# Kernel tuning notes

Hardware: AMD Instinct MI355X
Metric: run time of the kernel (lower is better)

The kernel has to match this reference:

```python
import jax, jax.numpy as jnp
import numpy as np

B, T, C = 2, 2048, 1024
H = 16
D = C // H  # head_dim = 64


def setup_inputs() -> dict:
    key = jax.random.key(0)
    k1, k2, k3, k4 = jax.random.split(key, 4)
    x = jax.random.normal(k1, (B, T, C), dtype=jnp.float32)
    # parameter scales ~ torch default init magnitude
    w_qkv = jax.random.normal(k2, (C, 3 * C), dtype=jnp.float32) * (1.0 / np.sqrt(C))
    w_proj = jax.random.normal(k3, (C, C), dtype=jnp.float32) * (1.0 / np.sqrt(C))
    b_proj = jax.random.normal(k4, (C,), dtype=jnp.float32) * 0.01
    return {"x": x, "w_qkv": w_qkv, "w_proj": w_proj, "b_proj": b_proj}


def reference(x, w_qkv, w_proj, b_proj):
    b, t, c = x.shape
    scale = 1.0 / jnp.sqrt(jnp.asarray(D, dtype=x.dtype))
    qkv = x @ w_qkv                                   # [B,T,3C]
    q, k, v = jnp.split(qkv, 3, axis=-1)
    def heads(u):  # [B,T,C] -> [B,H,T,D]
        return u.reshape(b, t, H, D).transpose(0, 2, 1, 3)
    q, k, v = heads(q), heads(k), heads(v)
    attn = jnp.einsum('bhqd,bhkd->bhqk', q, k) * scale  # [B,H,T,T]
    causal = jnp.tril(jnp.ones((t, t), dtype=bool))
    attn = jnp.where(causal, attn, -jnp.inf)
    attn = jax.nn.softmax(attn, axis=-1)
    # dropout p=0.0 / eval mode: identity
    out = jnp.einsum('bhqk,bhkd->bhqd', attn, v)        # [B,H,T,D]
    out = out.transpose(0, 2, 1, 3).reshape(b, t, c)
    return out @ w_proj + b_proj
```

## Files before the change

### kernel.cpp

```cpp
#include <hip/hip_runtime.h>
#include <stdint.h>

#define Bn 2
#define Tn 2048
#define Cn 1024
#define Hn 16
#define Dn 64
#define Mn (Bn*Tn)

typedef __attribute__((ext_vector_type(8))) short bf16x8;
typedef __attribute__((ext_vector_type(4))) float f32x4;
typedef __attribute__((ext_vector_type(4))) unsigned int u32x4;
typedef __attribute__((ext_vector_type(2))) unsigned int u32x2;
typedef unsigned short u16;

__device__ __forceinline__ u16 f2bf(float f) {
  union { float f; uint32_t u; } v; v.f = f;
  uint32_t u = v.u;
  return (u16)((u + 0x7fffu + ((u >> 16) & 1u)) >> 16);
}

__device__ __forceinline__ uint32_t pk_bf16(float lo, float hi) {
  uint32_t r;
  asm volatile("v_cvt_pk_bf16_f32 %0, %1, %2" : "=v"(r) : "v"(lo), "v"(hi));
  return r;
}

__device__ __forceinline__ void async16(const void* g, void* lds) {
  __builtin_amdgcn_global_load_lds((const __attribute__((address_space(1))) void*)g,
                                   (__attribute__((address_space(3))) void*)lds,
                                   16, 0, 0);
}


__global__ void cvt_x(const float* __restrict__ x, u16* __restrict__ xb) {
  int i = (blockIdx.x * 256 + threadIdx.x) * 4;
  float4 v = *(const float4*)(x + i);
  ushort4 o;
  o.x = f2bf(v.x); o.y = f2bf(v.y); o.z = f2bf(v.z); o.w = f2bf(v.w);
  *(ushort4*)(xb + i) = o;
}

template<int K, int N>
__global__ void cvt_T(const float* __restrict__ in, u16* __restrict__ out) {
  __shared__ float tile[32][33];
  int n0 = blockIdx.x * 32, k0 = blockIdx.y * 32;
  int tx = threadIdx.x & 31, ty = threadIdx.x >> 5;
  #pragma unroll
  for (int i = 0; i < 32; i += 8)
    tile[ty + i][tx] = in[(size_t)(k0 + ty + i) * N + n0 + tx];
  __syncthreads();
  #pragma unroll
  for (int i = 0; i < 32; i += 8)
    out[(size_t)(n0 + ty + i) * K + k0 + tx] = f2bf(tile[tx][ty + i]);
}


template<int EPI>
__launch_bounds__(256, 2)
__global__ void gemm_bt(const u16* __restrict__ A, const u16* __restrict__ Bt, int N,
                        u16* __restrict__ Qb, u16* __restrict__ Kb, u16* __restrict__ Vb,
                        float* __restrict__ Out, const float* __restrict__ bias) {
  constexpr int Kd = 1024;
  __shared__ u16 As[128][64];
  __shared__ u16 Bs[128][64];
  const int nT = N >> 7;
  const int m0 = (blockIdx.x / nT) << 7;
  const int n0 = (blockIdx.x % nT) << 7;
  const int tid = threadIdx.x;
  const int lane = tid & 63, wid = tid >> 6;
  const int wr = wid >> 1, wc = wid & 1;
  const int lr = lane & 15, lg = lane >> 4;

  f32x4 acc[4][4] = {};

  for (int kb = 0; kb < Kd; kb += 64) {
    #pragma unroll
    for (int i = 0; i < 4; ++i) {
      int c = (wid * 4 + i) * 64 + lane;
      int row = c >> 3, ko = (c & 7) << 3;
      async16(A + (size_t)(m0 + row) * Kd + kb + ko, &As[0][0] + c * 8);
      async16(Bt + (size_t)(n0 + row) * Kd + kb + ko, &Bs[0][0] + c * 8);
    }
    __syncthreads();
    bf16x8 af[2][4], bf[2][4];
    #pragma unroll
    for (int kc = 0; kc < 2; ++kc) {
      #pragma unroll
      for (int mi = 0; mi < 4; ++mi) {
        af[kc][mi] = *(const bf16x8*)&As[wr * 64 + mi * 16 + lr][kc * 32 + lg * 8];
        bf[kc][mi] = *(const bf16x8*)&Bs[wc * 64 + mi * 16 + lr][kc * 32 + lg * 8];
      }
    }
    #pragma unroll
    for (int kc = 0; kc < 2; ++kc)
      #pragma unroll
      for (int mi = 0; mi < 4; ++mi)
        #pragma unroll
        for (int ni = 0; ni < 4; ++ni)
          acc[mi][ni] = __builtin_amdgcn_mfma_f32_16x16x32_bf16(af[kc][mi], bf[kc][ni], acc[mi][ni], 0, 0, 0);
    __syncthreads();
  }

  if constexpr (EPI == 0) {
    #pragma unroll
    for (int mi = 0; mi < 4; ++mi) {
      int r0 = m0 + wr * 64 + mi * 16 + lg * 4;
      int bb = r0 >> 11;
      int t0 = r0 & 2047;
      #pragma unroll
      for (int ni = 0; ni < 4; ++ni) {
        int col = n0 + wc * 64 + ni * 16 + lr;
        int sel = col >> 10, rem = col & 1023;
        int h = rem >> 6, d = rem & 63;
        f32x4 v = acc[mi][ni];
        if (sel == 0) {
          size_t base = ((size_t)(bb * Hn + h) * Tn + t0) * Dn + d;
          #pragma unroll
          for (int r = 0; r < 4; ++r) Qb[base + (size_t)r * Dn] = f2bf(v[r] * 0.125f);
        } else if (sel == 1) {
          size_t base = ((size_t)(bb * Hn + h) * Tn + t0) * Dn + d;
          #pragma unroll
          for (int r = 0; r < 4; ++r) Kb[base + (size_t)r * Dn] = f2bf(v[r]);
        } else {
          size_t base = ((size_t)(bb * Hn + h) * Dn + d) * Tn + t0;
          ushort4 o;
          o.x = f2bf(v[0]); o.y = f2bf(v[1]); o.z = f2bf(v[2]); o.w = f2bf(v[3]);
          *(ushort4*)(Vb + base) = o;
        }
      }
    }
  } else {
    #pragma unroll
    for (int mi = 0; mi < 4; ++mi) {
      int r0 = m0 + wr * 64 + mi * 16 + lg * 4;
      #pragma unroll
      for (int ni = 0; ni < 4; ++ni) {
        int col = n0 + wc * 64 + ni * 16 + lr;
        float bv = bias[col];
        #pragma unroll
        for (int r = 0; r < 4; ++r)
          Out[(size_t)(r0 + r) * Cn + col] = acc[mi][ni][r] + bv;
      }
    }
  }
}


__device__ __forceinline__ void stage_kv(const u16* __restrict__ K,
                                         const u16* __restrict__ Vt, int k0,
                                         u16* __restrict__ Kbuf, u16* __restrict__ Vbuf,
                                         int tid) {
  #pragma unroll
  for (int i = 0; i < 2; ++i) {
    int c = i * 256 + tid;
    int row = c >> 3;
    int js = (c & 7) ^ (row & 7);
    async16(K + (size_t)(k0 + row) * Dn + js * 8, Kbuf + c * 8);
    async16(Vt + (size_t)row * Tn + k0 + js * 8, Vbuf + c * 8);
  }
}

__launch_bounds__(256, 2)
__global__ void attn(const u16* __restrict__ Qb, const u16* __restrict__ Kb,
                     const u16* __restrict__ Vb, u16* __restrict__ Ob) {
  __shared__ u16 __attribute__((aligned(16))) Ks[2 * 4096];
  __shared__ u16 __attribute__((aligned(16))) Vs[2 * 4096];
  __shared__ uint32_t __attribute__((aligned(16))) P32[4][16][36];

  const int x = blockIdx.x;
  const int wg = (x & 7) * 64 + (x >> 3);
  const int bh = wg >> 4;
  const int a  = wg & 15;
  const int tid = threadIdx.x;
  const int lane = tid & 63, wid = tid >> 6;
  const int lr = lane & 15, lg = lane >> 4;
  const int bb = bh >> 4, h = bh & 15;

  const u16* Q  = Qb + (size_t)bh * Tn * Dn;
  const u16* K  = Kb + (size_t)bh * Tn * Dn;
  const u16* Vt = Vb + (size_t)bh * Dn * Tn;

  const int swz = (lr & 7);
  const int qoff = wid * 16 + lr;
  const int koff0 = lg * 4;

  #pragma unroll 1
  for (int g = 0; g < 2; ++g) {
    const int q0 = (g == 0 ? (31 - a) : a) * 64;
    const int nt = (q0 >> 6) + 1;

    bf16x8 qf[2];
    qf[0] = *(const bf16x8*)(Q + (size_t)(q0 + qoff) * Dn + lg * 8);
    qf[1] = *(const bf16x8*)(Q + (size_t)(q0 + qoff) * Dn + 32 + lg * 8);

    f32x4 o[4] = {};
    float m = -1e30f, l = 0.f;

    int cur = 0;
    stage_kv(K, Vt, 0, Ks, Vs, tid);
    __syncthreads();

    for (int t = 0; t < nt; ++t) {
      if (t + 1 < nt)
        stage_kv(K, Vt, (t + 1) << 6,
                 Ks + (cur ^ 1) * 4096, Vs + (cur ^ 1) * 4096, tid);

      const u16* Kc = Ks + cur * 4096;
      const u16* Vc = Vs + cur * 4096;

      f32x4 s[4] = {};
      __builtin_amdgcn_s_setprio(1);
      #pragma unroll
      for (int f = 0; f < 4; ++f) {
        const int row = f * 16 + lr;
        #pragma unroll
        for (int kc = 0; kc < 2; ++kc) {
          bf16x8 kf = *(const bf16x8*)(Kc + row * 64 + (((kc * 4 + lg) ^ swz) * 8));
          s[f] = __builtin_amdgcn_mfma_f32_16x16x32_bf16(kf, qf[kc], s[f], 0, 0, 0);
        }
      }
      __builtin_amdgcn_s_setprio(0);

      if (t == nt - 1) {
        #pragma unroll
        for (int f = 0; f < 4; ++f)
          #pragma unroll
          for (int r = 0; r < 4; ++r)
            if (f * 16 + koff0 + r > qoff) s[f][r] = -1e30f;
      }

      float pm = fmaxf(fmaxf(fmaxf(s[0][0], s[0][1]), fmaxf(s[0][2], s[0][3])),
                       fmaxf(fmaxf(s[1][0], s[1][1]), fmaxf(s[1][2], s[1][3])));
      float pm2 = fmaxf(fmaxf(fmaxf(s[2][0], s[2][1]), fmaxf(s[2][2], s[2][3])),
                        fmaxf(fmaxf(s[3][0], s[3][1]), fmaxf(s[3][2], s[3][3])));
      pm = fmaxf(pm, pm2);
      pm = fmaxf(pm, __shfl_xor(pm, 16));
      pm = fmaxf(pm, __shfl_xor(pm, 32));

      if (!__all(pm - m <= 8.f)) {
        float mn = fmaxf(m, pm);
        float fac = __expf(m - mn);
        l *= fac;
        #pragma unroll
        for (int f = 0; f < 4; ++f) {
          o[f][0] *= fac; o[f][1] *= fac; o[f][2] *= fac; o[f][3] *= fac;
        }
        m = mn;
      }

      float sum = 0.f;
      #pragma unroll
      for (int f = 0; f < 4; ++f) {
        #pragma unroll
        for (int r = 0; r < 4; ++r) {
          float p = __expf(s[f][r] - m);
          s[f][r] = p;
          sum += p;
        }
      }
      sum += __shfl_xor(sum, 16);
      sum += __shfl_xor(sum, 32);
      l += sum;

      #pragma unroll
      for (int f = 0; f < 4; ++f) {
        u32x2 w;
        w.x = pk_bf16(s[f][0], s[f][1]);
        w.y = pk_bf16(s[f][2], s[f][3]);
        *(u32x2*)&P32[wid][lr][f * 8 + lg * 2] = w;
      }

      __builtin_amdgcn_s_setprio(1);
      #pragma unroll
      for (int kc = 0; kc < 2; ++kc) {
        u32x4 p4 = *(const u32x4*)&P32[wid][lr][kc * 16 + lg * 4];
        bf16x8 pf = __builtin_bit_cast(bf16x8, p4);
        #pragma unroll
        for (int f = 0; f < 4; ++f) {
          const int row = f * 16 + lr;
          bf16x8 vf = *(const bf16x8*)(Vc + row * 64 + (((kc * 4 + lg) ^ swz) * 8));
          o[f] = __builtin_amdgcn_mfma_f32_16x16x32_bf16(vf, pf, o[f], 0, 0, 0);
        }
      }
      __builtin_amdgcn_s_setprio(0);

      __syncthreads();
      cur ^= 1;
    }

    float inv = 1.f / l;
    #pragma unroll
    for (int f = 0; f < 4; ++f) {
      u32x2 w;
      w.x = pk_bf16(o[f][0] * inv, o[f][1] * inv);
      w.y = pk_bf16(o[f][2] * inv, o[f][3] * inv);
      *(u32x2*)&P32[wid][lr][f * 8 + lg * 2] = w;
    }
    u32x4 r0 = *(const u32x4*)&P32[wid][lr][lg * 8];
    u32x4 r1 = *(const u32x4*)&P32[wid][lr][lg * 8 + 4];
    u16* obase = Ob + ((size_t)(bb * Tn + q0 + qoff)) * Cn + h * Dn + lg * 16;
    *(u32x4*)(obase) = r0;
    *(u32x4*)(obase + 8) = r1;
    __syncthreads();
  }
}


extern "C" void kernel_launch(void* const* d_in, const int* in_sizes, int n_in,
                              void* d_out, int out_size, void* d_ws, size_t ws_size,
                              hipStream_t stream) {
  const float* x = (const float*)d_in[0];
  const float* w_qkv = (const float*)d_in[1];
  const float* w_proj = (const float*)d_in[2];
  const float* b_proj = (const float*)d_in[3];
  float* out = (float*)d_out;
  char* ws = (char*)d_ws;

  u16* xb     = (u16*)(ws);
  u16* wqkvT  = (u16*)(ws + (size_t)( 8u << 20));
  u16* wprojT = (u16*)(ws + (size_t)(14u << 20));
  u16* Qb     = (u16*)(ws + (size_t)(16u << 20));
  u16* Kb     = (u16*)(ws + (size_t)(24u << 20));
  u16* Vb     = (u16*)(ws + (size_t)(32u << 20));

  cvt_x<<<dim3(4096), dim3(256), 0, stream>>>(x, xb);
  cvt_T<1024, 3072><<<dim3(96, 32), dim3(256), 0, stream>>>(w_qkv, wqkvT);
  cvt_T<1024, 1024><<<dim3(32, 32), dim3(256), 0, stream>>>(w_proj, wprojT);

  gemm_bt<0><<<dim3(32 * 24), dim3(256), 0, stream>>>(xb, wqkvT, 3072,
                                                      Qb, Kb, Vb, nullptr, nullptr);
  attn<<<dim3(512), dim3(256), 0, stream>>>(Qb, Kb, Vb, xb );
  gemm_bt<1><<<dim3(32 * 8), dim3(256), 0, stream>>>(xb, wprojT, 1024,
                                                     nullptr, nullptr, nullptr, out, b_proj);
}
```

Before: 122.2 us.

## Load V directly to registers, split attention grid per query tile, raise occupancy

The attention kernel no longer stages V through shared memory; each wave loads its V fragments straight from global memory into registers, which halves the LDS footprint. Launch bounds go from 2 to 4 blocks per CU, and the grid doubles to one block per (batch-head, query tile) instead of pairing long and short tiles in one block. Blocks are ordered longest-first and grouped so that each XCD handles four heads. The intent is more concurrent waves to hide latency, at the cost of redundant uncoalesced global V reads across the four waves and more register pressure.

```diff
diff --git a/kernel.cpp b/kernel.cpp
--- a/kernel.cpp
+++ b/kernel.cpp
@@ -147,31 +147,31 @@
 }
 
 
-__device__ __forceinline__ void stage_kv(const u16* __restrict__ K,
-                                         const u16* __restrict__ Vt, int k0,
-                                         u16* __restrict__ Kbuf, u16* __restrict__ Vbuf,
-                                         int tid) {
+__device__ __forceinline__ void stage_k(const u16* __restrict__ K, int k0,
+                                        u16* __restrict__ Kbuf, int tid) {
   #pragma unroll
   for (int i = 0; i < 2; ++i) {
     int c = i * 256 + tid;
     int row = c >> 3;
     int js = (c & 7) ^ (row & 7);
     async16(K + (size_t)(k0 + row) * Dn + js * 8, Kbuf + c * 8);
-    async16(Vt + (size_t)row * Tn + k0 + js * 8, Vbuf + c * 8);
-  }
-}
-
-__launch_bounds__(256, 2)
+  }
+}
+
+__launch_bounds__(256, 4)
 __global__ void attn(const u16* __restrict__ Qb, const u16* __restrict__ Kb,
                      const u16* __restrict__ Vb, u16* __restrict__ Ob) {
   __shared__ u16 __attribute__((aligned(16))) Ks[2 * 4096];
-  __shared__ u16 __attribute__((aligned(16))) Vs[2 * 4096];
   __shared__ uint32_t __attribute__((aligned(16))) P32[4][16][36];
 
-  const int x = blockIdx.x;
-  const int wg = (x & 7) * 64 + (x >> 3);
-  const int bh = wg >> 4;
-  const int a  = wg & 15;
+  const int raw = blockIdx.x;
+  const int xcd = raw & 7;
+  const int idx = raw >> 3;
+  const int bh  = xcd * 4 + (idx & 3);
+  const int qt  = 31 - (idx >> 2);
+  const int q0  = qt * 64;
+  const int nt  = qt + 1;
+
   const int tid = threadIdx.x;
   const int lane = tid & 63, wid = tid >> 6;
   const int lr = lane & 15, lg = lane >> 4;
@@ -185,125 +185,121 @@
   const int qoff = wid * 16 + lr;
   const int koff0 = lg * 4;
 
-  #pragma unroll 1
-  for (int g = 0; g < 2; ++g) {
-    const int q0 = (g == 0 ? (31 - a) : a) * 64;
-    const int nt = (q0 >> 6) + 1;
-
-    bf16x8 qf[2];
-    qf[0] = *(const bf16x8*)(Q + (size_t)(q0 + qoff) * Dn + lg * 8);
-    qf[1] = *(const bf16x8*)(Q + (size_t)(q0 + qoff) * Dn + 32 + lg * 8);
-
-    f32x4 o[4] = {};
-    float m = -1e30f, l = 0.f;
-
-    int cur = 0;
-    stage_kv(K, Vt, 0, Ks, Vs, tid);
-    __syncthreads();
-
-    for (int t = 0; t < nt; ++t) {
-      if (t + 1 < nt)
-        stage_kv(K, Vt, (t + 1) << 6,
-                 Ks + (cur ^ 1) * 4096, Vs + (cur ^ 1) * 4096, tid);
-
-      const u16* Kc = Ks + cur * 4096;
-      const u16* Vc = Vs + cur * 4096;
-
-      f32x4 s[4] = {};
-      __builtin_amdgcn_s_setprio(1);
+  bf16x8 qf[2];
+  qf[0] = *(const bf16x8*)(Q + (size_t)(q0 + qoff) * Dn + lg * 8);
+  qf[1] = *(const bf16x8*)(Q + (size_t)(q0 + qoff) * Dn + 32 + lg * 8);
+
+  f32x4 o[4] = {};
+  float m = -1e30f, l = 0.f;
+
+  int cur = 0;
+  stage_k(K, 0, Ks, tid);
+  __syncthreads();
+
+  for (int t = 0; t < nt; ++t) {
+    const int k0 = t << 6;
+    if (t + 1 < nt)
+      stage_k(K, (t + 1) << 6, Ks + (cur ^ 1) * 4096, tid);
+
+    bf16x8 vf[2][4];
+    #pragma unroll
+    for (int kc = 0; kc < 2; ++kc)
+      #pragma unroll
+      for (int f = 0; f < 4; ++f)
+        vf[kc][f] = *(const bf16x8*)(Vt + (size_t)(f * 16 + lr) * Tn + k0 + kc * 32 + lg * 8);
+
+    const u16* Kc = Ks + cur * 4096;
+
+    f32x4 s[4] = {};
+    __builtin_amdgcn_s_setprio(1);
+    #pragma unroll
+    for (int f = 0; f < 4; ++f) {
+      const int row = f * 16 + lr;
+      #pragma unroll
+      for (int kc = 0; kc < 2; ++kc) {
+        bf16x8 kf = *(const bf16x8*)(Kc + row * 64 + (((kc * 4 + lg) ^ swz) * 8));
+        s[f] = __builtin_amdgcn_mfma_f32_16x16x32_bf16(kf, qf[kc], s[f], 0, 0, 0);
+      }
+    }
+    __builtin_amdgcn_s_setprio(0);
+
+    if (t == nt - 1) {
+      #pragma unroll
+      for (int f = 0; f < 4; ++f)
+        #pragma unroll
+        for (int r = 0; r < 4; ++r)
+          if (f * 16 + koff0 + r > qoff) s[f][r] = -1e30f;
+    }
+
+    float pm = fmaxf(fmaxf(fmaxf(s[0][0], s[0][1]), fmaxf(s[0][2], s[0][3])),
+                     fmaxf(fmaxf(s[1][0], s[1][1]), fmaxf(s[1][2], s[1][3])));
+    float pm2 = fmaxf(fmaxf(fmaxf(s[2][0], s[2][1]), fmaxf(s[2][2], s[2][3])),
+                      fmaxf(fmaxf(s[3][0], s[3][1]), fmaxf(s[3][2], s[3][3])));
+    pm = fmaxf(pm, pm2);
+    pm = fmaxf(pm, __shfl_xor(pm, 16));
+    pm = fmaxf(pm, __shfl_xor(pm, 32));
+
+    if (!__all(pm - m <= 8.f)) {
+      float mn = fmaxf(m, pm);
+      float fac = __expf(m - mn);
+      l *= fac;
       #pragma unroll
       for (int f = 0; f < 4; ++f) {
-        const int row = f * 16 + lr;
-        #pragma unroll
-        for (int kc = 0; kc < 2; ++kc) {
-          bf16x8 kf = *(const bf16x8*)(Kc + row * 64 + (((kc * 4 + lg) ^ swz) * 8));
-          s[f] = __builtin_amdgcn_mfma_f32_16x16x32_bf16(kf, qf[kc], s[f], 0, 0, 0);
-        }
-      }
-      __builtin_amdgcn_s_setprio(0);
-
-      if (t == nt - 1) {
-        #pragma unroll
-        for (int f = 0; f < 4; ++f)
-          #pragma unroll
-          for (int r = 0; r < 4; ++r)
-            if (f * 16 + koff0 + r > qoff) s[f][r] = -1e30f;
-      }
-
-      float pm = fmaxf(fmaxf(fmaxf(s[0][0], s[0][1]), fmaxf(s[0][2], s[0][3])),
-                       fmaxf(fmaxf(s[1][0], s[1][1]), fmaxf(s[1][2], s[1][3])));
-      float pm2 = fmaxf(fmaxf(fmaxf(s[2][0], s[2][1]), fmaxf(s[2][2], s[2][3])),
-                        fmaxf(fmaxf(s[3][0], s[3][1]), fmaxf(s[3][2], s[3][3])));
-      pm = fmaxf(pm, pm2);
-      pm = fmaxf(pm, __shfl_xor(pm, 16));
-      pm = fmaxf(pm, __shfl_xor(pm, 32));
-
-      if (!__all(pm - m <= 8.f)) {
-        float mn = fmaxf(m, pm);
-        float fac = __expf(m - mn);
-        l *= fac;
-        #pragma unroll
-        for (int f = 0; f < 4; ++f) {
-          o[f][0] *= fac; o[f][1] *= fac; o[f][2] *= fac; o[f][3] *= fac;
-        }
-        m = mn;
-      }
-
-      float sum = 0.f;
-      #pragma unroll
-      for (int f = 0; f < 4; ++f) {
-        #pragma unroll
-        for (int r = 0; r < 4; ++r) {
-          float p = __expf(s[f][r] - m);
-          s[f][r] = p;
-          sum += p;
-        }
-      }
-      sum += __shfl_xor(sum, 16);
-      sum += __shfl_xor(sum, 32);
-      l += sum;
-
-      #pragma unroll
-      for (int f = 0; f < 4; ++f) {
-        u32x2 w;
-        w.x = pk_bf16(s[f][0], s[f][1]);
-        w.y = pk_bf16(s[f][2], s[f][3]);
-        *(u32x2*)&P32[wid][lr][f * 8 + lg * 2] = w;
-      }
-
-      __builtin_amdgcn_s_setprio(1);
-      #pragma unroll
-      for (int kc = 0; kc < 2; ++kc) {
-        u32x4 p4 = *(const u32x4*)&P32[wid][lr][kc * 16 + lg * 4];
-        bf16x8 pf = __builtin_bit_cast(bf16x8, p4);
-        #pragma unroll
-        for (int f = 0; f < 4; ++f) {
-          const int row = f * 16 + lr;
-          bf16x8 vf = *(const bf16x8*)(Vc + row * 64 + (((kc * 4 + lg) ^ swz) * 8));
-          o[f] = __builtin_amdgcn_mfma_f32_16x16x32_bf16(vf, pf, o[f], 0, 0, 0);
-        }
-      }
-      __builtin_amdgcn_s_setprio(0);
-
-      __syncthreads();
-      cur ^= 1;
-    }
-
-    float inv = 1.f / l;
+        o[f][0] *= fac; o[f][1] *= fac; o[f][2] *= fac; o[f][3] *= fac;
+      }
+      m = mn;
+    }
+
+    float sum = 0.f;
+    #pragma unroll
+    for (int f = 0; f < 4; ++f) {
+      #pragma unroll
+      for (int r = 0; r < 4; ++r) {
+        float p = __expf(s[f][r] - m);
+        s[f][r] = p;
+        sum += p;
+      }
+    }
+    sum += __shfl_xor(sum, 16);
+    sum += __shfl_xor(sum, 32);
+    l += sum;
+
     #pragma unroll
     for (int f = 0; f < 4; ++f) {
       u32x2 w;
-      w.x = pk_bf16(o[f][0] * inv, o[f][1] * inv);
-      w.y = pk_bf16(o[f][2] * inv, o[f][3] * inv);
+      w.x = pk_bf16(s[f][0], s[f][1]);
+      w.y = pk_bf16(s[f][2], s[f][3]);
       *(u32x2*)&P32[wid][lr][f * 8 + lg * 2] = w;
     }
-    u32x4 r0 = *(const u32x4*)&P32[wid][lr][lg * 8];
-    u32x4 r1 = *(const u32x4*)&P32[wid][lr][lg * 8 + 4];
-    u16* obase = Ob + ((size_t)(bb * Tn + q0 + qoff)) * Cn + h * Dn + lg * 16;
-    *(u32x4*)(obase) = r0;
-    *(u32x4*)(obase + 8) = r1;
+
+    __builtin_amdgcn_s_setprio(1);
+    #pragma unroll
+    for (int kc = 0; kc < 2; ++kc) {
+      u32x4 p4 = *(const u32x4*)&P32[wid][lr][kc * 16 + lg * 4];
+      bf16x8 pf = __builtin_bit_cast(bf16x8, p4);
+      #pragma unroll
+      for (int f = 0; f < 4; ++f)
+        o[f] = __builtin_amdgcn_mfma_f32_16x16x32_bf16(vf[kc][f], pf, o[f], 0, 0, 0);
+    }
+    __builtin_amdgcn_s_setprio(0);
+
     __syncthreads();
-  }
+    cur ^= 1;
+  }
+
+  float inv = 1.f / l;
+  #pragma unroll
+  for (int f = 0; f < 4; ++f) {
+    u32x2 w;
+    w.x = pk_bf16(o[f][0] * inv, o[f][1] * inv);
+    w.y = pk_bf16(o[f][2] * inv, o[f][3] * inv);
+    *(u32x2*)&P32[wid][lr][f * 8 + lg * 2] = w;
+  }
+  u32x4 r0 = *(const u32x4*)&P32[wid][lr][lg * 8];
+  u32x4 r1 = *(const u32x4*)&P32[wid][lr][lg * 8 + 4];
+  u16* obase = Ob + ((size_t)(bb * Tn + q0 + qoff)) * Cn + h * Dn + lg * 16;
+  *(u32x4*)(obase) = r0;
+  *(u32x4*)(obase + 8) = r1;
 }
 
 
@@ -330,7 +326,7 @@
 
   gemm_bt<0><<<dim3(32 * 24), dim3(256), 0, stream>>>(xb, wqkvT, 3072,
                                                       Qb, Kb, Vb, nullptr, nullptr);
-  attn<<<dim3(512), dim3(256), 0, stream>>>(Qb, Kb, Vb, xb );
+  attn<<<dim3(1024), dim3(256), 0, stream>>>(Qb, Kb, Vb, xb );
   gemm_bt<1><<<dim3(32 * 8), dim3(256), 0, stream>>>(xb, wprojT, 1024,
                                                      nullptr, nullptr, nullptr, out, b_proj);
 }
```

Measured after the change: 163.1 us. +33.5%, slower.
